# Performance work log

Measured on AMD Instinct MI355X. Metric: run time of the kernel, lower is better.

The kernel has to match this reference:

```python
import jax, jax.numpy as jnp
import numpy as np

GRU_H, H1, H2, ODIM = 256, 128, 64, 3
B, T, HOP = 16, 4000, 80
N = T * HOP  # 320000 samples


def setup_inputs() -> dict:
    key = jax.random.key(0)
    ks = jax.random.split(key, 12)
    inp = {
        'gru_output': jax.random.normal(ks[0], (B, T, GRU_H), dtype=jnp.float32),
        'enhanced': jax.random.normal(ks[1], (B, N), dtype=jnp.float32) * 0.3,
        'noisy': None,
        'W1': jax.random.normal(ks[3], (H1, GRU_H), dtype=jnp.float32) * 0.05,
        'b1': jnp.zeros((H1,), dtype=jnp.float32),
        'a1': jnp.asarray(0.25, dtype=jnp.float32),
        'W2': jax.random.normal(ks[4], (H2, H1), dtype=jnp.float32) * 0.08,
        'b2': jnp.zeros((H2,), dtype=jnp.float32),
        'a2': jnp.asarray(0.25, dtype=jnp.float32),
        'W3': jax.random.normal(ks[5], (ODIM, H2), dtype=jnp.float32) * 0.1,
        'b3': jnp.zeros((ODIM,), dtype=jnp.float32),
    }
    inp['noisy'] = inp['enhanced'] + jax.random.normal(ks[2], (B, N), dtype=jnp.float32) * 0.1
    return inp


def _prelu(x, a):
    return jnp.where(x >= 0, x, a * x)


def _interp_linear(x, n_out):
    # torch F.interpolate(mode='linear', align_corners=False): x [B, T] -> [B, n_out]
    t = x.shape[1]
    src = (jnp.arange(n_out, dtype=jnp.float32) + 0.5) * (t / n_out) - 0.5
    src = jnp.clip(src, 0.0, t - 1)
    i0 = jnp.floor(src).astype(jnp.int32)
    i1 = jnp.minimum(i0 + 1, t - 1)
    w = src - i0.astype(jnp.float32)
    return x[:, i0] * (1.0 - w) + x[:, i1] * w


def _compress(audio, ratio, threshold):
    # soft-knee static gain followed by single-pole IIR smoothing (alpha=0.1)
    env = jnp.abs(audio)
    gain_red = jnp.where(env > threshold, threshold + (env - threshold) / ratio, env)
    gain = jnp.clip(gain_red / (env + 1e-8), 0.1, 2.0)
    alpha = 0.1
    g0 = gain[:, 0]

    def step(carry, g):
        s = alpha * g + (1.0 - alpha) * carry
        return s, s

    _, rest = jax.lax.scan(step, g0, gain[:, 1:].T)  # scan over time, carry [B]
    smoothed = jnp.concatenate([g0[:, None], rest.T], axis=1)
    return audio * smoothed


def reference(gru_output, enhanced, noisy, W1, b1, a1, W2, b2, a2, W3, b3):
    # params MLP (dropout = identity in eval)
    h = _prelu(jnp.einsum('bth,oh->bto', gru_output, W1) + b1, a1)
    h = _prelu(jnp.einsum('bth,oh->bto', h, W2) + b2, a2)
    p = jnp.einsum('bth,oh->bto', h, W3) + b3  # [B, T, 3]

    attack = jax.nn.sigmoid(p[..., 0]) * 0.019 + 0.001
    release = jax.nn.sigmoid(p[..., 1]) * 0.19 + 0.01
    ratio = jnp.clip(jax.nn.softplus(p[..., 2]) + 1.0, 1.0, 20.0)

    n = enhanced.shape[1]
    ratio_i = _interp_linear(ratio, n)
    # attack/release are interpolated in the original but unused by _apply_compression
    _ = _interp_linear(attack, n)
    _ = _interp_linear(release, n)

    residual = noisy - enhanced
    comp_enh = _compress(enhanced, ratio_i, 0.3)
    comp_res = _compress(residual, ratio_i * 0.5, 0.1)

    out = comp_enh + 0.1 * comp_res
    out = out / (jnp.max(jnp.abs(out)) + 1e-8) * jnp.max(jnp.abs(enhanced))
    return out
```

## Files before the change

kernel.cpp:

```cpp
#include <hip/hip_runtime.h>
#include <hip/hip_bf16.h>
#include <math.h>

#define GRU_H 256
#define H1D   128
#define H2D   64
#define BB    16
#define TT    4000
#define NN    320000

typedef __attribute__((ext_vector_type(8))) short short8;
typedef __attribute__((ext_vector_type(4))) float f32x4;

static __device__ __forceinline__ unsigned short f2bf(float x) {
    __bf16 b = (__bf16)x;
    return __builtin_bit_cast(unsigned short, b);
}
static __device__ __forceinline__ float bf2f(unsigned short h) {
    return __uint_as_float(((unsigned)h) << 16);
}

#define WS_ESLOT 1024

#define H1CH 4608
#define W2CH 2304
__global__ __launch_bounds__(256) void mlp_kernel(
    const float* __restrict__ gru, const float* __restrict__ W1,
    const float* __restrict__ b1,  const float* __restrict__ a1p,
    const float* __restrict__ W2,  const float* __restrict__ b2,
    const float* __restrict__ a2p, const float* __restrict__ W3,
    const float* __restrict__ b3,  float* __restrict__ ratio_out,
    unsigned* __restrict__ ws_u)
{
    __shared__ unsigned short smem[36864];
    __shared__ float w3f[64];
    unsigned short* As  = smem;
    unsigned short* Bs  = smem + 4608;
    unsigned short* h2s = smem;
    unsigned short* h1s = smem + 9216;
    unsigned short* W2s = smem + 27648;

    const int t    = threadIdx.x;
    const int wave = t >> 6, lane = t & 63;
    const int lr   = lane & 15, q = lane >> 4;
    const int m0   = blockIdx.x * 128;
    const float a1v = a1p[0], a2v = a2p[0];

    if (blockIdx.x == 0) {
        #pragma unroll
        for (int i = t; i < 2048; i += 256) ws_u[i] = 0u;
    }
    if (t < 64) w3f[t] = W3[2 * H2D + t];

    const int wr = wave >> 1;
    const int wc = wave & 1;
    f32x4 acc1[4][4];
    #pragma unroll
    for (int mi = 0; mi < 4; ++mi)
        #pragma unroll
        for (int ni = 0; ni < 4; ++ni) acc1[mi][ni] = (f32x4){0.f, 0.f, 0.f, 0.f};

    for (int kc = 0; kc < 8; ++kc) {
        const int k0 = kc * 32;
        __syncthreads();
        #pragma unroll
        for (int it = 0; it < 4; ++it) {
            const int idx = t + 256 * it;
            const int row = idx >> 3, c4 = idx & 7;
            float4 g = *(const float4*)(gru + (size_t)(m0 + row) * GRU_H + k0 + c4 * 4);
            ushort4 gh = {f2bf(g.x), f2bf(g.y), f2bf(g.z), f2bf(g.w)};
            *(ushort4*)(As + row * 36 + c4 * 4) = gh;
            float4 w = *(const float4*)(W1 + (size_t)row * GRU_H + k0 + c4 * 4);
            ushort4 wh = {f2bf(w.x), f2bf(w.y), f2bf(w.z), f2bf(w.w)};
            *(ushort4*)(Bs + row * 36 + c4 * 4) = wh;
        }
        __syncthreads();
        short8 af[4], bf[4];
        #pragma unroll
        for (int mi = 0; mi < 4; ++mi) {
            const unsigned short* p = As + (wr * 64 + mi * 16 + lr) * 36 + q * 8;
            ushort4 lo = *(const ushort4*)(p), hi = *(const ushort4*)(p + 4);
            af[mi] = (short8){(short)lo.x, (short)lo.y, (short)lo.z, (short)lo.w,
                              (short)hi.x, (short)hi.y, (short)hi.z, (short)hi.w};
        }
        #pragma unroll
        for (int ni = 0; ni < 4; ++ni) {
            const unsigned short* p = Bs + (wc * 64 + ni * 16 + lr) * 36 + q * 8;
            ushort4 lo = *(const ushort4*)(p), hi = *(const ushort4*)(p + 4);
            bf[ni] = (short8){(short)lo.x, (short)lo.y, (short)lo.z, (short)lo.w,
                              (short)hi.x, (short)hi.y, (short)hi.z, (short)hi.w};
        }
        #pragma unroll
        for (int mi = 0; mi < 4; ++mi)
            #pragma unroll
            for (int ni = 0; ni < 4; ++ni)
                acc1[mi][ni] = __builtin_amdgcn_mfma_f32_16x16x32_bf16(
                    af[mi], bf[ni], acc1[mi][ni], 0, 0, 0);
    }

    #pragma unroll
    for (int ni = 0; ni < 4; ++ni) {
        const int col = wc * 64 + ni * 16 + lr;
        const float bv = b1[col];
        unsigned short* dst = h1s + (col >> 5) * H1CH + (col & 31);
        #pragma unroll
        for (int mi = 0; mi < 4; ++mi) {
            const int rbase = wr * 64 + mi * 16 + q * 4;
            #pragma unroll
            for (int r = 0; r < 4; ++r) {
                float x = acc1[mi][ni][r] + bv;
                x = (x >= 0.f) ? x : a1v * x;
                dst[(rbase + r) * 36] = f2bf(x);
            }
        }
    }
    #pragma unroll
    for (int it = 0; it < 8; ++it) {
        const int idx = t + 256 * it;
        const int row = idx >> 5, c4 = idx & 31;
        float4 w = *(const float4*)(W2 + (size_t)row * H1D + c4 * 4);
        ushort4 wh = {f2bf(w.x), f2bf(w.y), f2bf(w.z), f2bf(w.w)};
        *(ushort4*)(W2s + (c4 >> 3) * W2CH + row * 36 + (c4 & 7) * 4) = wh;
    }
    __syncthreads();

    const int wr2 = wave >> 1;
    const int wc2 = wave & 1;
    f32x4 acc2[4][2];
    #pragma unroll
    for (int mi = 0; mi < 4; ++mi)
        #pragma unroll
        for (int ni = 0; ni < 2; ++ni) acc2[mi][ni] = (f32x4){0.f, 0.f, 0.f, 0.f};

    #pragma unroll
    for (int kc = 0; kc < 4; ++kc) {
        short8 af[4], bf[2];
        #pragma unroll
        for (int mi = 0; mi < 4; ++mi) {
            const unsigned short* p = h1s + kc * H1CH + (wr2 * 64 + mi * 16 + lr) * 36 + q * 8;
            ushort4 lo = *(const ushort4*)(p), hi = *(const ushort4*)(p + 4);
            af[mi] = (short8){(short)lo.x, (short)lo.y, (short)lo.z, (short)lo.w,
                              (short)hi.x, (short)hi.y, (short)hi.z, (short)hi.w};
        }
        #pragma unroll
        for (int ni = 0; ni < 2; ++ni) {
            const unsigned short* p = W2s + kc * W2CH + (wc2 * 32 + ni * 16 + lr) * 36 + q * 8;
            ushort4 lo = *(const ushort4*)(p), hi = *(const ushort4*)(p + 4);
            bf[ni] = (short8){(short)lo.x, (short)lo.y, (short)lo.z, (short)lo.w,
                              (short)hi.x, (short)hi.y, (short)hi.z, (short)hi.w};
        }
        #pragma unroll
        for (int mi = 0; mi < 4; ++mi)
            #pragma unroll
            for (int ni = 0; ni < 2; ++ni)
                acc2[mi][ni] = __builtin_amdgcn_mfma_f32_16x16x32_bf16(
                    af[mi], bf[ni], acc2[mi][ni], 0, 0, 0);
    }

    #pragma unroll
    for (int ni = 0; ni < 2; ++ni) {
        const int col = wc2 * 32 + ni * 16 + lr;
        const float bv = b2[col];
        unsigned short* dst = h2s + (col >> 5) * H1CH + (col & 31);
        #pragma unroll
        for (int mi = 0; mi < 4; ++mi) {
            const int rbase = wr2 * 64 + mi * 16 + q * 4;
            #pragma unroll
            for (int r = 0; r < 4; ++r) {
                float x = acc2[mi][ni][r] + bv;
                x = (x >= 0.f) ? x : a2v * x;
                dst[(rbase + r) * 36] = f2bf(x);
            }
        }
    }
    __syncthreads();

    if (t < 128) {
        float p = b3[2];
        #pragma unroll
        for (int k = 0; k < 64; ++k)
            p = fmaf(bf2f(h2s[(k >> 5) * H1CH + t * 36 + (k & 31)]), w3f[k], p);
        float sp = fmaxf(p, 0.f) + log1pf(expf(-fabsf(p)));
        ratio_out[m0 + t] = fminf(sp + 1.0f, 20.0f);
    }
}

#define CH     256
#define SEGCH  5
#define SEGLEN (CH * SEGCH)
#define SPR    (NN / SEGLEN)
#define NBLK   (BB * SPR / 4)

__global__ __launch_bounds__(256, 4) void compress_kernel(
    const float* __restrict__ enh_g, const float* __restrict__ noi_g,
    const float* __restrict__ ratio, float* __restrict__ out,
    unsigned* __restrict__ ws_u)
{
    const int lane = threadIdx.x & 63;
    const int wid  = blockIdx.x * 4 + (threadIdx.x >> 6);
    const int row  = wid / SPR;
    const int seg  = wid - row * SPR;
    const int s0   = seg * SEGLEN;

    const float* __restrict__ enh  = enh_g + (size_t)row * NN;
    const float* __restrict__ noi  = noi_g + (size_t)row * NN;
    const float* __restrict__ rrow = ratio + row * TT;
    float* __restrict__ orow       = out   + (size_t)row * NN;

    float d_lane = 1.f;
    if (lane & 1)  d_lane *= 0.65610000f;
    if (lane & 2)  d_lane *= 0.43046721f;
    if (lane & 4)  d_lane *= 0.18530202f;
    if (lane & 8)  d_lane *= 0.034336838f;
    if (lane & 16) d_lane *= 0.0011790185f;
    if (lane & 32) d_lane *= 1.3900845e-06f;

    const int p0w = s0 - CH + 4 * lane;
    const int pcw = p0w < 0 ? 0 : p0w;
    float4 e_cur = *(const float4*)(enh + pcw);
    float4 x_cur = *(const float4*)(noi + pcw);

    float s_e = 0.f, s_r = 0.f;
    float amax_c = 0.f, amax_e = 0.f;

    #pragma unroll
    for (int ci = 0; ci < SEGCH + 1; ++ci) {
        float4 e_nxt, x_nxt;
        if (ci < SEGCH) {
            const int pn = s0 - CH + (ci + 1) * CH + 4 * lane;
            e_nxt = *(const float4*)(enh + pn);
            x_nxt = *(const float4*)(noi + pn);
        }

        const int cb = s0 - CH + ci * CH;
        const int p0 = cb + 4 * lane;

        float pe[4], pr[4];
        float ge0 = 0.f, gr0 = 0.f;
        float ae = 0.f, ar = 0.f;
        #pragma unroll
        for (int k = 0; k < 4; ++k) {
            const float e   = (&e_cur.x)[k];
            const float x   = (&x_cur.x)[k];
            const float res = x - e;
            const int n  = p0 + k;
            const int nc = n < 0 ? 0 : n;
            float src = fmaf((float)nc + 0.5f, 0.0125f, -0.5f);
            src = fminf(fmaxf(src, 0.f), 3999.f);
            const int   i0 = (int)src;
            const float w  = src - (float)i0;
            const int   i1 = min(i0 + 1, 3999);
            const float r0 = rrow[i0], r1 = rrow[i1];
            const float rr = r0 * (1.f - w) + r1 * w;
            const float rcp_rr = __builtin_amdgcn_rcpf(rr);

            const float env_e = fabsf(e);
            const float gre = (env_e > 0.3f) ? fmaf(env_e - 0.3f, rcp_rr, 0.3f) : env_e;
            const float ge  = fminf(fmaxf(gre * __builtin_amdgcn_rcpf(env_e + 1e-8f), 0.1f), 2.f);
            const float env_r = fabsf(res);
            const float grr = (env_r > 0.1f) ? fmaf(env_r - 0.1f, 2.f * rcp_rr, 0.1f) : env_r;
            const float gr  = fminf(fmaxf(grr * __builtin_amdgcn_rcpf(env_r + 1e-8f), 0.1f), 2.f);

            if (k == 0) { ge0 = ge; gr0 = gr; }
            ae = fmaf(0.9f, ae, 0.1f * ge);
            ar = fmaf(0.9f, ar, 0.1f * gr);
            pe[k] = ae; pr[k] = ar;
        }

        float Be = pe[3], Br = pr[3];
        #pragma unroll
        for (int l = 0; l < 6; ++l) {
            const int dlt = 1 << l;
            const float ml = (l == 0) ? 0.65610000f  :
                             (l == 1) ? 0.43046721f  :
                             (l == 2) ? 0.18530202f  :
                             (l == 3) ? 0.034336838f :
                             (l == 4) ? 0.0011790185f : 1.3900845e-06f;
            const float me  = (lane >= dlt) ? ml : 0.f;
            const float bse = __shfl_up(Be, dlt, 64);
            const float bsr = __shfl_up(Br, dlt, 64);
            Be = fmaf(me, bse, Be);
            Br = fmaf(me, bsr, Br);
        }
        float Ee = __shfl_up(Be, 1, 64); if (lane == 0) Ee = 0.f;
        float Er = __shfl_up(Br, 1, 64); if (lane == 0) Er = 0.f;

        if (cb == 0) { s_e = __shfl(ge0, 0, 64); s_r = __shfl(gr0, 0, 64); }

        const float Se = fmaf(d_lane, s_e, Ee);
        const float Sr = fmaf(d_lane, s_r, Er);

        if (ci > 0) {
            float4 o;
            #pragma unroll
            for (int k = 0; k < 4; ++k) {
                const float ck = (k == 0) ? 0.9f : (k == 1) ? 0.81f
                               : (k == 2) ? 0.729f : 0.6561f;
                const float sek = fmaf(ck, Se, pe[k]);
                const float srk = fmaf(ck, Sr, pr[k]);
                const float e   = (&e_cur.x)[k];
                const float res = (&x_cur.x)[k] - e;
                const float c   = fmaf(0.1f * res, srk, e * sek);
                (&o.x)[k] = c;
                amax_c = fmaxf(amax_c, fabsf(c));
                amax_e = fmaxf(amax_e, fabsf(e));
            }
            *(float4*)(orow + p0) = o;
        }

        const float b63e = __shfl(Be, 63, 64);
        const float b63r = __shfl(Br, 63, 64);
        s_e = fmaf(1.9287e-12f, s_e, b63e);
        s_r = fmaf(1.9287e-12f, s_r, b63r);
        e_cur = e_nxt; x_cur = x_nxt;
    }

    #pragma unroll
    for (int off = 32; off > 0; off >>= 1) {
        amax_c = fmaxf(amax_c, __shfl_xor(amax_c, off, 64));
        amax_e = fmaxf(amax_e, __shfl_xor(amax_e, off, 64));
    }
    __shared__ float red[8];
    const int wv = threadIdx.x >> 6, ln = threadIdx.x & 63;
    if (ln == 0) { red[wv] = amax_c; red[4 + wv] = amax_e; }
    __syncthreads();
    if (threadIdx.x == 0) {
        float mc = fmaxf(fmaxf(red[0], red[1]), fmaxf(red[2], red[3]));
        float me = fmaxf(fmaxf(red[4], red[5]), fmaxf(red[6], red[7]));
        const int slot = (blockIdx.x & 63) * 16;
        atomicMax(ws_u + slot, __float_as_uint(mc));
        atomicMax(ws_u + WS_ESLOT + slot, __float_as_uint(me));
    }
}

__global__ __launch_bounds__(256) void scale_kernel(float4* __restrict__ out4,
                                                    const unsigned* __restrict__ ws_u)
{
    const int lane = threadIdx.x & 63;
    float vc = __uint_as_float(ws_u[lane * 16]);
    float ve = __uint_as_float(ws_u[WS_ESLOT + lane * 16]);
    #pragma unroll
    for (int off = 32; off > 0; off >>= 1) {
        vc = fmaxf(vc, __shfl_xor(vc, off, 64));
        ve = fmaxf(ve, __shfl_xor(ve, off, 64));
    }
    const float scale = ve / (vc + 1e-8f);
    const size_t i = (size_t)blockIdx.x * 256 + threadIdx.x;
    float4 v = out4[i];
    v.x *= scale; v.y *= scale; v.z *= scale; v.w *= scale;
    out4[i] = v;
}

extern "C" void kernel_launch(void* const* d_in, const int* in_sizes, int n_in,
                              void* d_out, int out_size, void* d_ws, size_t ws_size,
                              hipStream_t stream) {
    const float* gru = (const float*)d_in[0];
    const float* enh = (const float*)d_in[1];
    const float* noi = (const float*)d_in[2];
    const float* W1  = (const float*)d_in[3];
    const float* b1  = (const float*)d_in[4];
    const float* a1  = (const float*)d_in[5];
    const float* W2  = (const float*)d_in[6];
    const float* b2  = (const float*)d_in[7];
    const float* a2  = (const float*)d_in[8];
    const float* W3  = (const float*)d_in[9];
    const float* b3  = (const float*)d_in[10];
    float* out = (float*)d_out;

    unsigned* ws_u = (unsigned*)d_ws;
    float* ratio   = (float*)((char*)d_ws + 8192);

    mlp_kernel<<<(BB * TT) / 128, 256, 0, stream>>>(gru, W1, b1, a1, W2, b2, a2, W3, b3, ratio, ws_u);
    compress_kernel<<<NBLK, 256, 0, stream>>>(enh, noi, ratio, out, ws_u);
    scale_kernel<<<(BB * NN) / 4 / 256, 256, 0, stream>>>((float4*)out, ws_u);
}
```

Before: 174.5 us.

## Load MLP MFMA fragments directly from global memory instead of LDS staging

The GEMM1 and GEMM2 operands (gru, W1, W2) are now loaded straight from global memory into per-lane MFMA fragments with bf16 conversion in registers. This removes the LDS staging tiles for A/B and W2 and the two barriers per k-chunk in the first GEMM. LDS drops to the h1/h2 buffers, which can raise occupancy. In exchange, each wave re-reads operands that other waves share (W1 and the gru rows are read redundantly, relying on L1/L2), and the global accesses are less coalesced 32-byte per-lane reads.

Measured after the change: 188.8 us. +8.2%, slower.

```diff
diff --git a/kernel.cpp b/kernel.cpp
--- a/kernel.cpp
+++ b/kernel.cpp
@@ -19,11 +19,16 @@
 static __device__ __forceinline__ float bf2f(unsigned short h) {
     return __uint_as_float(((unsigned)h) << 16);
 }
+static __device__ __forceinline__ short8 load_frag8(const float* __restrict__ p) {
+    float4 lo = *(const float4*)(p);
+    float4 hi = *(const float4*)(p + 4);
+    return (short8){(short)f2bf(lo.x), (short)f2bf(lo.y), (short)f2bf(lo.z), (short)f2bf(lo.w),
+                    (short)f2bf(hi.x), (short)f2bf(hi.y), (short)f2bf(hi.z), (short)f2bf(hi.w)};
+}
 
 #define WS_ESLOT 1024
 
 #define H1CH 4608
-#define W2CH 2304
 __global__ __launch_bounds__(256) void mlp_kernel(
     const float* __restrict__ gru, const float* __restrict__ W1,
     const float* __restrict__ b1,  const float* __restrict__ a1p,
@@ -32,13 +37,10 @@
     const float* __restrict__ b3,  float* __restrict__ ratio_out,
     unsigned* __restrict__ ws_u)
 {
-    __shared__ unsigned short smem[36864];
+    __shared__ unsigned short smem[27648];
     __shared__ float w3f[64];
-    unsigned short* As  = smem;
-    unsigned short* Bs  = smem + 4608;
-    unsigned short* h2s = smem;
-    unsigned short* h1s = smem + 9216;
-    unsigned short* W2s = smem + 27648;
+    unsigned short* h1s = smem;
+    unsigned short* h2s = smem + 18432;
 
     const int t    = threadIdx.x;
     const int wave = t >> 6, lane = t & 63;
@@ -60,36 +62,19 @@
         #pragma unroll
         for (int ni = 0; ni < 4; ++ni) acc1[mi][ni] = (f32x4){0.f, 0.f, 0.f, 0.f};
 
+    const float* ga = gru + (size_t)(m0 + wr * 64 + lr) * GRU_H + q * 8;
+    const float* wb = W1  + (size_t)(wc * 64 + lr) * GRU_H + q * 8;
+
+    #pragma unroll
     for (int kc = 0; kc < 8; ++kc) {
         const int k0 = kc * 32;
-        __syncthreads();
-        #pragma unroll
-        for (int it = 0; it < 4; ++it) {
-            const int idx = t + 256 * it;
-            const int row = idx >> 3, c4 = idx & 7;
-            float4 g = *(const float4*)(gru + (size_t)(m0 + row) * GRU_H + k0 + c4 * 4);
-            ushort4 gh = {f2bf(g.x), f2bf(g.y), f2bf(g.z), f2bf(g.w)};
-            *(ushort4*)(As + row * 36 + c4 * 4) = gh;
-            float4 w = *(const float4*)(W1 + (size_t)row * GRU_H + k0 + c4 * 4);
-            ushort4 wh = {f2bf(w.x), f2bf(w.y), f2bf(w.z), f2bf(w.w)};
-            *(ushort4*)(Bs + row * 36 + c4 * 4) = wh;
-        }
-        __syncthreads();
         short8 af[4], bf[4];
         #pragma unroll
-        for (int mi = 0; mi < 4; ++mi) {
-            const unsigned short* p = As + (wr * 64 + mi * 16 + lr) * 36 + q * 8;
-            ushort4 lo = *(const ushort4*)(p), hi = *(const ushort4*)(p + 4);
-            af[mi] = (short8){(short)lo.x, (short)lo.y, (short)lo.z, (short)lo.w,
-                              (short)hi.x, (short)hi.y, (short)hi.z, (short)hi.w};
-        }
-        #pragma unroll
-        for (int ni = 0; ni < 4; ++ni) {
-            const unsigned short* p = Bs + (wc * 64 + ni * 16 + lr) * 36 + q * 8;
-            ushort4 lo = *(const ushort4*)(p), hi = *(const ushort4*)(p + 4);
-            bf[ni] = (short8){(short)lo.x, (short)lo.y, (short)lo.z, (short)lo.w,
-                              (short)hi.x, (short)hi.y, (short)hi.z, (short)hi.w};
-        }
+        for (int mi = 0; mi < 4; ++mi)
+            af[mi] = load_frag8(ga + (size_t)(mi * 16) * GRU_H + k0);
+        #pragma unroll
+        for (int ni = 0; ni < 4; ++ni)
+            bf[ni] = load_frag8(wb + (size_t)(ni * 16) * GRU_H + k0);
         #pragma unroll
         for (int mi = 0; mi < 4; ++mi)
             #pragma unroll
@@ -114,14 +99,6 @@
             }
         }
     }
-    #pragma unroll
-    for (int it = 0; it < 8; ++it) {
-        const int idx = t + 256 * it;
-        const int row = idx >> 5, c4 = idx & 31;
-        float4 w = *(const float4*)(W2 + (size_t)row * H1D + c4 * 4);
-        ushort4 wh = {f2bf(w.x), f2bf(w.y), f2bf(w.z), f2bf(w.w)};
-        *(ushort4*)(W2s + (c4 >> 3) * W2CH + row * 36 + (c4 & 7) * 4) = wh;
-    }
     __syncthreads();
 
     const int wr2 = wave >> 1;
@@ -131,6 +108,8 @@
     for (int mi = 0; mi < 4; ++mi)
         #pragma unroll
         for (int ni = 0; ni < 2; ++ni) acc2[mi][ni] = (f32x4){0.f, 0.f, 0.f, 0.f};
+
+    const float* w2b = W2 + (size_t)(wc2 * 32 + lr) * H1D + q * 8;
 
     #pragma unroll
     for (int kc = 0; kc < 4; ++kc) {
@@ -143,12 +122,8 @@
                               (short)hi.x, (short)hi.y, (short)hi.z, (short)hi.w};
         }
         #pragma unroll
-        for (int ni = 0; ni < 2; ++ni) {
-            const unsigned short* p = W2s + kc * W2CH + (wc2 * 32 + ni * 16 + lr) * 36 + q * 8;
-            ushort4 lo = *(const ushort4*)(p), hi = *(const ushort4*)(p + 4);
-            bf[ni] = (short8){(short)lo.x, (short)lo.y, (short)lo.z, (short)lo.w,
-                              (short)hi.x, (short)hi.y, (short)hi.z, (short)hi.w};
-        }
+        for (int ni = 0; ni < 2; ++ni)
+            bf[ni] = load_frag8(w2b + (size_t)(ni * 16) * H1D + kc * 32);
         #pragma unroll
         for (int mi = 0; mi < 4; ++mi)
             #pragma unroll
```

## Register-prefetch next K chunk of GRU and W1 tiles during MFMA loop

Applied to the files above, without the earlier changes.

The first GEMM loop now loads the next 32-wide K chunk of gru_output and W1 into registers before the barrier, while the current chunk sits in LDS and the MFMAs run. This is software pipelining meant to hide global memory latency behind compute. Launch bounds also ask for 2 blocks per SM, which caps register use; the extra prefetch registers could spill or lower occupancy.

New measurement: 172.0 us, median of 2. Within noise of the previous version (-1.4%).

```diff
diff --git a/kernel.cpp b/kernel.cpp
--- a/kernel.cpp
+++ b/kernel.cpp
@@ -19,12 +19,15 @@
 static __device__ __forceinline__ float bf2f(unsigned short h) {
     return __uint_as_float(((unsigned)h) << 16);
 }
+static __device__ __forceinline__ ushort4 cvt4(float4 v) {
+    return (ushort4){f2bf(v.x), f2bf(v.y), f2bf(v.z), f2bf(v.w)};
+}
 
 #define WS_ESLOT 1024
 
 #define H1CH 4608
 #define W2CH 2304
-__global__ __launch_bounds__(256) void mlp_kernel(
+__global__ __launch_bounds__(256, 2) void mlp_kernel(
     const float* __restrict__ gru, const float* __restrict__ W1,
     const float* __restrict__ b1,  const float* __restrict__ a1p,
     const float* __restrict__ W2,  const float* __restrict__ b2,
@@ -60,21 +63,36 @@
         #pragma unroll
         for (int ni = 0; ni < 4; ++ni) acc1[mi][ni] = (f32x4){0.f, 0.f, 0.f, 0.f};
 
+    const int srow[4] = { (t + 0)   >> 3, (t + 256) >> 3,
+                          (t + 512) >> 3, (t + 768) >> 3 };
+    const int sc4 = t & 7;
+
+    float4 rg[4], rw[4];
+    #pragma unroll
+    for (int it = 0; it < 4; ++it) {
+        rg[it] = *(const float4*)(gru + (size_t)(m0 + srow[it]) * GRU_H + sc4 * 4);
+        rw[it] = *(const float4*)(W1  + (size_t)srow[it] * GRU_H + sc4 * 4);
+    }
+
+    #pragma unroll 1
     for (int kc = 0; kc < 8; ++kc) {
-        const int k0 = kc * 32;
         __syncthreads();
         #pragma unroll
         for (int it = 0; it < 4; ++it) {
-            const int idx = t + 256 * it;
-            const int row = idx >> 3, c4 = idx & 7;
-            float4 g = *(const float4*)(gru + (size_t)(m0 + row) * GRU_H + k0 + c4 * 4);
-            ushort4 gh = {f2bf(g.x), f2bf(g.y), f2bf(g.z), f2bf(g.w)};
-            *(ushort4*)(As + row * 36 + c4 * 4) = gh;
-            float4 w = *(const float4*)(W1 + (size_t)row * GRU_H + k0 + c4 * 4);
-            ushort4 wh = {f2bf(w.x), f2bf(w.y), f2bf(w.z), f2bf(w.w)};
-            *(ushort4*)(Bs + row * 36 + c4 * 4) = wh;
+            *(ushort4*)(As + srow[it] * 36 + sc4 * 4) = cvt4(rg[it]);
+            *(ushort4*)(Bs + srow[it] * 36 + sc4 * 4) = cvt4(rw[it]);
+        }
+        float4 ng[4], nw[4];
+        if (kc < 7) {
+            const int k1 = (kc + 1) * 32;
+            #pragma unroll
+            for (int it = 0; it < 4; ++it) {
+                ng[it] = *(const float4*)(gru + (size_t)(m0 + srow[it]) * GRU_H + k1 + sc4 * 4);
+                nw[it] = *(const float4*)(W1  + (size_t)srow[it] * GRU_H + k1 + sc4 * 4);
+            }
         }
         __syncthreads();
+
         short8 af[4], bf[4];
         #pragma unroll
         for (int mi = 0; mi < 4; ++mi) {
@@ -96,6 +114,11 @@
             for (int ni = 0; ni < 4; ++ni)
                 acc1[mi][ni] = __builtin_amdgcn_mfma_f32_16x16x32_bf16(
                     af[mi], bf[ni], acc1[mi][ni], 0, 0, 0);
+
+        if (kc < 7) {
+            #pragma unroll
+            for (int it = 0; it < 4; ++it) { rg[it] = ng[it]; rw[it] = nw[it]; }
+        }
     }
 
     #pragma unroll
@@ -119,8 +142,7 @@
         const int idx = t + 256 * it;
         const int row = idx >> 5, c4 = idx & 31;
         float4 w = *(const float4*)(W2 + (size_t)row * H1D + c4 * 4);
-        ushort4 wh = {f2bf(w.x), f2bf(w.y), f2bf(w.z), f2bf(w.w)};
-        *(ushort4*)(W2s + (c4 >> 3) * W2CH + row * 36 + (c4 & 7) * 4) = wh;
+        *(ushort4*)(W2s + (c4 >> 3) * W2CH + row * 36 + (c4 & 7) * 4) = cvt4(w);
     }
     __syncthreads();
 
```

## Shrink MLP row tile to 64, prefetch next K-chunk into registers, load W2 fragments directly

Applied to the files above, without the earlier changes.

The MLP kernel now processes 64 rows per block instead of 128, which cuts shared memory from about 72KB to about 32KB and sets launch_bounds to allow 4 blocks per CU. The block count doubles to 1000. The next K-chunk of gru and W1 is prefetched into registers while MFMAs run on the current chunk, overlapping global loads with compute. W2 is no longer staged through LDS; each wave loads its B fragments straight from global memory and converts them to bf16. The trade-off is that W1 is reloaded by twice as many blocks and each block does less work to amortise it.

Result: no change. 174.9 us (+0.3%).

```diff
diff --git a/kernel.cpp b/kernel.cpp
--- a/kernel.cpp
+++ b/kernel.cpp
@@ -19,12 +19,18 @@
 static __device__ __forceinline__ float bf2f(unsigned short h) {
     return __uint_as_float(((unsigned)h) << 16);
 }
+static __device__ __forceinline__ ushort4 cvt4(float4 v) {
+    return (ushort4){f2bf(v.x), f2bf(v.y), f2bf(v.z), f2bf(v.w)};
+}
+static __device__ __forceinline__ short8 cvt_frag(float4 lo, float4 hi) {
+    return (short8){(short)f2bf(lo.x), (short)f2bf(lo.y), (short)f2bf(lo.z), (short)f2bf(lo.w),
+                    (short)f2bf(hi.x), (short)f2bf(hi.y), (short)f2bf(hi.z), (short)f2bf(hi.w)};
+}
 
 #define WS_ESLOT 1024
 
-#define H1CH 4608
-#define W2CH 2304
-__global__ __launch_bounds__(256) void mlp_kernel(
+#define A1CH 2304
+__global__ __launch_bounds__(256, 4) void mlp_kernel(
     const float* __restrict__ gru, const float* __restrict__ W1,
     const float* __restrict__ b1,  const float* __restrict__ a1p,
     const float* __restrict__ W2,  const float* __restrict__ b2,
@@ -32,18 +38,17 @@
     const float* __restrict__ b3,  float* __restrict__ ratio_out,
     unsigned* __restrict__ ws_u)
 {
-    __shared__ unsigned short smem[36864];
+    __shared__ unsigned short smem[16128];
     __shared__ float w3f[64];
     unsigned short* As  = smem;
-    unsigned short* Bs  = smem + 4608;
+    unsigned short* Bs  = smem + 2304;
+    unsigned short* h1s = smem + 6912;
     unsigned short* h2s = smem;
-    unsigned short* h1s = smem + 9216;
-    unsigned short* W2s = smem + 27648;
 
     const int t    = threadIdx.x;
     const int wave = t >> 6, lane = t & 63;
     const int lr   = lane & 15, q = lane >> 4;
-    const int m0   = blockIdx.x * 128;
+    const int m0   = blockIdx.x * 64;
     const float a1v = a1p[0], a2v = a2p[0];
 
     if (blockIdx.x == 0) {
@@ -52,40 +57,54 @@
     }
     if (t < 64) w3f[t] = W3[2 * H2D + t];
 
-    const int wr = wave >> 1;
-    const int wc = wave & 1;
-    f32x4 acc1[4][4];
+    f32x4 acc1[4][2];
     #pragma unroll
     for (int mi = 0; mi < 4; ++mi)
         #pragma unroll
-        for (int ni = 0; ni < 4; ++ni) acc1[mi][ni] = (f32x4){0.f, 0.f, 0.f, 0.f};
-
+        for (int ni = 0; ni < 2; ++ni) acc1[mi][ni] = (f32x4){0.f, 0.f, 0.f, 0.f};
+
+    const int arow0 = t >> 3, arow1 = (t + 256) >> 3;
+    const int sc4   = t & 7;
+    const int brow[4] = { t >> 3, (t + 256) >> 3, (t + 512) >> 3, (t + 768) >> 3 };
+
+    float4 rg[2], rw[4];
+    rg[0] = *(const float4*)(gru + (size_t)(m0 + arow0) * GRU_H + sc4 * 4);
+    rg[1] = *(const float4*)(gru + (size_t)(m0 + arow1) * GRU_H + sc4 * 4);
+    #pragma unroll
+    for (int it = 0; it < 4; ++it)
+        rw[it] = *(const float4*)(W1 + (size_t)brow[it] * GRU_H + sc4 * 4);
+
+    #pragma unroll 1
     for (int kc = 0; kc < 8; ++kc) {
-        const int k0 = kc * 32;
         __syncthreads();
-        #pragma unroll
-        for (int it = 0; it < 4; ++it) {
-            const int idx = t + 256 * it;
-            const int row = idx >> 3, c4 = idx & 7;
-            float4 g = *(const float4*)(gru + (size_t)(m0 + row) * GRU_H + k0 + c4 * 4);
-            ushort4 gh = {f2bf(g.x), f2bf(g.y), f2bf(g.z), f2bf(g.w)};
-            *(ushort4*)(As + row * 36 + c4 * 4) = gh;
-            float4 w = *(const float4*)(W1 + (size_t)row * GRU_H + k0 + c4 * 4);
-            ushort4 wh = {f2bf(w.x), f2bf(w.y), f2bf(w.z), f2bf(w.w)};
-            *(ushort4*)(Bs + row * 36 + c4 * 4) = wh;
+        *(ushort4*)(As + arow0 * 36 + sc4 * 4) = cvt4(rg[0]);
+        *(ushort4*)(As + arow1 * 36 + sc4 * 4) = cvt4(rg[1]);
+        #pragma unroll
+        for (int it = 0; it < 4; ++it)
+            *(ushort4*)(Bs + brow[it] * 36 + sc4 * 4) = cvt4(rw[it]);
+
+        float4 ng[2], nw[4];
+        if (kc < 7) {
+            const int k1 = (kc + 1) * 32;
+            ng[0] = *(const float4*)(gru + (size_t)(m0 + arow0) * GRU_H + k1 + sc4 * 4);
+            ng[1] = *(const float4*)(gru + (size_t)(m0 + arow1) * GRU_H + k1 + sc4 * 4);
+            #pragma unroll
+            for (int it = 0; it < 4; ++it)
+                nw[it] = *(const float4*)(W1 + (size_t)brow[it] * GRU_H + k1 + sc4 * 4);
         }
         __syncthreads();
-        short8 af[4], bf[4];
+
+        short8 af[4], bf[2];
         #pragma unroll
         for (int mi = 0; mi < 4; ++mi) {
-            const unsigned short* p = As + (wr * 64 + mi * 16 + lr) * 36 + q * 8;
+            const unsigned short* p = As + (mi * 16 + lr) * 36 + q * 8;
             ushort4 lo = *(const ushort4*)(p), hi = *(const ushort4*)(p + 4);
             af[mi] = (short8){(short)lo.x, (short)lo.y, (short)lo.z, (short)lo.w,
                               (short)hi.x, (short)hi.y, (short)hi.z, (short)hi.w};
         }
         #pragma unroll
-        for (int ni = 0; ni < 4; ++ni) {
-            const unsigned short* p = Bs + (wc * 64 + ni * 16 + lr) * 36 + q * 8;
+        for (int ni = 0; ni < 2; ++ni) {
+            const unsigned short* p = Bs + (wave * 32 + ni * 16 + lr) * 36 + q * 8;
             ushort4 lo = *(const ushort4*)(p), hi = *(const ushort4*)(p + 4);
             bf[ni] = (short8){(short)lo.x, (short)lo.y, (short)lo.z, (short)lo.w,
                               (short)hi.x, (short)hi.y, (short)hi.z, (short)hi.w};
@@ -93,19 +112,34 @@
         #pragma unroll
         for (int mi = 0; mi < 4; ++mi)
             #pragma unroll
-            for (int ni = 0; ni < 4; ++ni)
+            for (int ni = 0; ni < 2; ++ni)
                 acc1[mi][ni] = __builtin_amdgcn_mfma_f32_16x16x32_bf16(
                     af[mi], bf[ni], acc1[mi][ni], 0, 0, 0);
-    }
-
-    #pragma unroll
-    for (int ni = 0; ni < 4; ++ni) {
-        const int col = wc * 64 + ni * 16 + lr;
+
+        if (kc < 7) {
+            rg[0] = ng[0]; rg[1] = ng[1];
+            #pragma unroll
+            for (int it = 0; it < 4; ++it) rw[it] = nw[it];
+        }
+    }
+
+    const int col2 = wave * 16 + lr;
+    float4 rw2[4][2];
+    #pragma unroll
+    for (int kc = 0; kc < 4; ++kc) {
+        const float* p = W2 + (size_t)col2 * H1D + kc * 32 + q * 8;
+        rw2[kc][0] = *(const float4*)(p);
+        rw2[kc][1] = *(const float4*)(p + 4);
+    }
+
+    #pragma unroll
+    for (int ni = 0; ni < 2; ++ni) {
+        const int col = wave * 32 + ni * 16 + lr;
         const float bv = b1[col];
-        unsigned short* dst = h1s + (col >> 5) * H1CH + (col & 31);
+        unsigned short* dst = h1s + (col >> 5) * A1CH + (col & 31);
         #pragma unroll
         for (int mi = 0; mi < 4; ++mi) {
-            const int rbase = wr * 64 + mi * 16 + q * 4;
+            const int rbase = mi * 16 + q * 4;
             #pragma unroll
             for (int r = 0; r < 4; ++r) {
                 float x = acc1[mi][ni][r] + bv;
@@ -114,60 +148,38 @@
             }
         }
     }
-    #pragma unroll
-    for (int it = 0; it < 8; ++it) {
-        const int idx = t + 256 * it;
-        const int row = idx >> 5, c4 = idx & 31;
-        float4 w = *(const float4*)(W2 + (size_t)row * H1D + c4 * 4);
-        ushort4 wh = {f2bf(w.x), f2bf(w.y), f2bf(w.z), f2bf(w.w)};
-        *(ushort4*)(W2s + (c4 >> 3) * W2CH + row * 36 + (c4 & 7) * 4) = wh;
-    }
     __syncthreads();
 
-    const int wr2 = wave >> 1;
-    const int wc2 = wave & 1;
-    f32x4 acc2[4][2];
-    #pragma unroll
-    for (int mi = 0; mi < 4; ++mi)
-        #pragma unroll
-        for (int ni = 0; ni < 2; ++ni) acc2[mi][ni] = (f32x4){0.f, 0.f, 0.f, 0.f};
+    f32x4 acc2[4];
+    #pragma unroll
+    for (int mi = 0; mi < 4; ++mi) acc2[mi] = (f32x4){0.f, 0.f, 0.f, 0.f};
 
     #pragma unroll
     for (int kc = 0; kc < 4; ++kc) {
-        short8 af[4], bf[2];
+        short8 af[4];
         #pragma unroll
         for (int mi = 0; mi < 4; ++mi) {
-            const unsigned short* p = h1s + kc * H1CH + (wr2 * 64 + mi * 16 + lr) * 36 + q * 8;
+            const unsigned short* p = h1s + kc * A1CH + (mi * 16 + lr) * 36 + q * 8;
             ushort4 lo = *(const ushort4*)(p), hi = *(const ushort4*)(p + 4);
             af[mi] = (short8){(short)lo.x, (short)lo.y, (short)lo.z, (short)lo.w,
                               (short)hi.x, (short)hi.y, (short)hi.z, (short)hi.w};
         }
-        #pragma unroll
-        for (int ni = 0; ni < 2; ++ni) {
-            const unsigned short* p = W2s + kc * W2CH + (wc2 * 32 + ni * 16 + lr) * 36 + q * 8;
-            ushort4 lo = *(const ushort4*)(p), hi = *(const ushort4*)(p + 4);
-            bf[ni] = (short8){(short)lo.x, (short)lo.y, (short)lo.z, (short)lo.w,
-                              (short)hi.x, (short)hi.y, (short)hi.z, (short)hi.w};
-        }
+        const short8 bf = cvt_frag(rw2[kc][0], rw2[kc][1]);
         #pragma unroll
         for (int mi = 0; mi < 4; ++mi)
-            #pragma unroll
-            for (int ni = 0; ni < 2; ++ni)
-                acc2[mi][ni] = __builtin_amdgcn_mfma_f32_16x16x32_bf16(
-                    af[mi], bf[ni], acc2[mi][ni], 0, 0, 0);
-    }
-
-    #pragma unroll
-    for (int ni = 0; ni < 2; ++ni) {
-        const int col = wc2 * 32 + ni * 16 + lr;
-        const float bv = b2[col];
-        unsigned short* dst = h2s + (col >> 5) * H1CH + (col & 31);
+            acc2[mi] = __builtin_amdgcn_mfma_f32_16x16x32_bf16(
+                af[mi], bf, acc2[mi], 0, 0, 0);
+    }
+
+    {
+        const float bv = b2[col2];
+        unsigned short* dst = h2s + (col2 >> 5) * A1CH + (col2 & 31);
         #pragma unroll
         for (int mi = 0; mi < 4; ++mi) {
-            const int rbase = wr2 * 64 + mi * 16 + q * 4;
+            const int rbase = mi * 16 + q * 4;
             #pragma unroll
             for (int r = 0; r < 4; ++r) {
-                float x = acc2[mi][ni][r] + bv;
+                float x = acc2[mi][r] + bv;
                 x = (x >= 0.f) ? x : a2v * x;
                 dst[(rbase + r) * 36] = f2bf(x);
             }
@@ -175,11 +187,11 @@
     }
     __syncthreads();
 
-    if (t < 128) {
+    if (t < 64) {
         float p = b3[2];
         #pragma unroll
         for (int k = 0; k < 64; ++k)
-            p = fmaf(bf2f(h2s[(k >> 5) * H1CH + t * 36 + (k & 31)]), w3f[k], p);
+            p = fmaf(bf2f(h2s[(k >> 5) * A1CH + t * 36 + (k & 31)]), w3f[k], p);
         float sp = fmaxf(p, 0.f) + log1pf(expf(-fabsf(p)));
         ratio_out[m0 + t] = fminf(sp + 1.0f, 20.0f);
     }
@@ -370,7 +382,7 @@
     unsigned* ws_u = (unsigned*)d_ws;
     float* ratio   = (float*)((char*)d_ws + 8192);
 
-    mlp_kernel<<<(BB * TT) / 128, 256, 0, stream>>>(gru, W1, b1, a1, W2, b2, a2, W3, b3, ratio, ws_u);
+    mlp_kernel<<<(BB * TT) / 64, 256, 0, stream>>>(gru, W1, b1, a1, W2, b2, a2, W3, b3, ratio, ws_u);
     compress_kernel<<<NBLK, 256, 0, stream>>>(enh, noi, ratio, out, ws_u);
     scale_kernel<<<(BB * NN) / 4 / 256, 256, 0, stream>>>((float4*)out, ws_u);
 }
```
